# Performance work log

Hardware: AMD Instinct MI355X
Metric: run time of the kernel (lower is better)

The kernel has to match this reference:

```python
import jax, jax.numpy as jnp
import numpy as np

N = 100_000      # nodes
F_IN = 256       # num_features
HID = 128        # args.hidden
C = 32           # num_classes
E = 1_600_000    # edges
EPS = 0.1        # AntiSymmetricConv epsilon
GAMMA = 0.1      # AntiSymmetricConv gamma


def setup_inputs() -> dict:
    key = jax.random.key(0)
    ks = jax.random.split(key, 10)
    def rn(k, shape, scale=0.05):
        return jax.random.normal(k, shape, dtype=jnp.float32) * scale
    x = jax.random.normal(ks[0], (N, F_IN), dtype=jnp.float32)
    edge_index = jax.random.randint(ks[1], (2, E), 0, N, dtype=jnp.int32)
    return {
        "x": x,
        "lin1_w": rn(ks[2], (HID, F_IN)), "lin1_b": jnp.zeros((HID,), jnp.float32),
        "lin2_w": rn(ks[3], (C, HID)),   "lin2_b": jnp.zeros((C,), jnp.float32),
        "W1": rn(ks[4], (HID, HID)), "phi1_w": rn(ks[5], (HID, HID)), "b1": jnp.zeros((HID,), jnp.float32),
        "W2": rn(ks[6], (C, C)),     "phi2_w": rn(ks[7], (C, C)),     "b2": jnp.zeros((C,), jnp.float32),
        "edge_index": edge_index,
    }


def gcn_norm(edge_index, n):
    # GCNConv default: add self-loops, symmetric D^-1/2 (A+I) D^-1/2 normalization
    loops = jnp.arange(n, dtype=edge_index.dtype)
    row = jnp.concatenate([edge_index[0], loops])  # source
    col = jnp.concatenate([edge_index[1], loops])  # target (aggregation)
    deg = jax.ops.segment_sum(jnp.ones(row.shape[0], jnp.float32), col, num_segments=n)
    dinv = jnp.where(deg > 0, jax.lax.rsqrt(deg), 0.0)
    return row, col, dinv[row] * dinv[col]


def gcn_conv(x, phi_w, row, col, norm):
    xw = x @ phi_w.T                                  # [N, d]
    msgs = norm[:, None] * xw[row]                    # [E+N, d] gather
    return jax.ops.segment_sum(msgs, col, num_segments=x.shape[0])  # scatter-add


def anti_symmetric_conv(x, row, col, norm, W, phi_w, b):
    d = W.shape[0]
    aw = W - W.T - GAMMA * jnp.eye(d, dtype=W.dtype)  # antisymmetric weight
    h = gcn_conv(x, phi_w, row, col, norm)            # phi(x, edge_index)
    h = jnp.tanh(x @ aw.T + h + b)
    return x + EPS * h                                # one Euler step (num_iters=1)


def reference(x, lin1_w, lin1_b, lin2_w, lin2_b, W1, phi1_w, b1, W2, phi2_w, b2, edge_index):
    row, col, norm = gcn_norm(edge_index, x.shape[0])
    h = jax.nn.relu(x @ lin1_w.T + lin1_b)            # dropout is identity in eval
    h = anti_symmetric_conv(h, row, col, norm, W1, phi1_w, b1)
    h = h @ lin2_w.T + lin2_b
    h = anti_symmetric_conv(h, row, col, norm, W2, phi2_w, b2)
    return jax.nn.log_softmax(h, axis=1)
```

## Files before the change

kernel.cpp:

```cpp
#include <hip/hip_runtime.h>
#include <hip/hip_bf16.h>
#include <math.h>

#define N_NODES 100000
#define F_IN    256
#define HID     128
#define NCLS    32
#define NEDGES  1600000
#define EPS_C   0.1f
#define GAMMA_C 0.1f

#define NBK   782
#define CHUNK 4096
#define NCH   391
#define BMAX  4096

typedef __attribute__((ext_vector_type(8))) short short8;
typedef __attribute__((ext_vector_type(4))) float floatx4;

__device__ __forceinline__ float bf2f(unsigned short u) {
    union { unsigned int u; float f; } c;
    c.u = ((unsigned int)u) << 16;
    return c.f;
}
__device__ __forceinline__ unsigned short f2bf(float f) {
    union { float f; unsigned int u; } c; c.f = f;
    unsigned int u = c.u;
    u += 0x7FFFu + ((u >> 16) & 1u);
    return (unsigned short)(u >> 16);
}

__device__ __forceinline__ float ldf(const void* p, size_t i, int md) {
    return md ? ((const float*)p)[i] : bf2f(((const unsigned short*)p)[i]);
}
__device__ __forceinline__ short8 ld8(const void* p, size_t i, int md) {
    if (md) {
        const float* q = (const float*)p + i;
        short8 r;
#pragma unroll
        for (int j = 0; j < 8; ++j) r[j] = (short)f2bf(q[j]);
        return r;
    }
    return *(const short8*)((const unsigned short*)p + i);
}

__global__ void k_detect(const unsigned short* __restrict__ x, int* __restrict__ mode) {
    __shared__ int cnt;
    if (threadIdx.x == 0) cnt = 0;
    __syncthreads();
    float v = fabsf(bf2f(x[2 * threadIdx.x]));
    if (v > 1e4f || !isfinite(v)) atomicAdd(&cnt, 1);
    __syncthreads();
    if (threadIdx.x == 0) *mode = (cnt >= 8) ? 1 : 0;
}

__global__ __launch_bounds__(256) void k_hist2(const int* __restrict__ ecol,
                                               int* __restrict__ hist, int e) {
    __shared__ int lh[NBK];
    for (int i = threadIdx.x; i < NBK; i += 256) lh[i] = 0;
    __syncthreads();
    int base = blockIdx.x * CHUNK;
    int lim = base + CHUNK; if (lim > e) lim = e;
    for (int i = base + threadIdx.x; i < lim; i += 256)
        atomicAdd(&lh[ecol[i] >> 7], 1);
    __syncthreads();
    for (int i = threadIdx.x; i < NBK; i += 256) hist[blockIdx.x * NBK + i] = lh[i];
}

__global__ __launch_bounds__(256) void k_tot(const int* __restrict__ hist, int* __restrict__ tot) {
    __shared__ int s[256];
    int b = blockIdx.x;
    int v = 0;
    for (int blk = threadIdx.x; blk < NCH; blk += 256) v += hist[blk * NBK + b];
    s[threadIdx.x] = v;
    __syncthreads();
#pragma unroll
    for (int off = 128; off > 0; off >>= 1) {
        if (threadIdx.x < off) s[threadIdx.x] += s[threadIdx.x + off];
        __syncthreads();
    }
    if (threadIdx.x == 0) tot[b] = s[0];
}

__global__ void k_bscan(const int* __restrict__ tot, int* __restrict__ bbase) {
    __shared__ int s[1024];
    int v = (threadIdx.x < NBK) ? tot[threadIdx.x] : 0;
    s[threadIdx.x] = v;
    __syncthreads();
#pragma unroll
    for (int off = 1; off < 1024; off <<= 1) {
        int t = (threadIdx.x >= off) ? s[threadIdx.x - off] : 0;
        __syncthreads();
        s[threadIdx.x] += t;
        __syncthreads();
    }
    if (threadIdx.x < NBK) bbase[threadIdx.x] = s[threadIdx.x] - v;
}

__global__ __launch_bounds__(512) void k_colscan(const int* __restrict__ hist,
                                                 const int* __restrict__ bbase,
                                                 int* __restrict__ off) {
    __shared__ int s[512];
    int b = blockIdx.x, t = threadIdx.x;
    int v = (t < NCH) ? hist[t * NBK + b] : 0;
    s[t] = v;
    __syncthreads();
#pragma unroll
    for (int o = 1; o < 512; o <<= 1) {
        int u = (t >= o) ? s[t - o] : 0;
        __syncthreads();
        s[t] += u;
        __syncthreads();
    }
    if (t < NCH) off[t * NBK + b] = s[t] - v + bbase[b];
}

__global__ __launch_bounds__(256) void k_pass3(
    const int* __restrict__ erow, const int* __restrict__ ecol,
    const int* __restrict__ off, unsigned int* __restrict__ pairs, int e)
{
    __shared__ int lh[NBK];
    __shared__ int lex[NBK + 1];
    __shared__ int cur[NBK];
    __shared__ int wsum[256];
    __shared__ unsigned int sp[CHUNK];
    int base = blockIdx.x * CHUNK;
    int lim = base + CHUNK; if (lim > e) lim = e;
    int cnt = lim - base;

    for (int i = threadIdx.x; i < NBK; i += 256) lh[i] = 0;
    __syncthreads();
    for (int i = base + threadIdx.x; i < lim; i += 256)
        atomicAdd(&lh[ecol[i] >> 7], 1);
    __syncthreads();

    int t4 = threadIdx.x * 4;
    int a0 = (t4 + 0 < NBK) ? lh[t4 + 0] : 0;
    int a1 = (t4 + 1 < NBK) ? lh[t4 + 1] : 0;
    int a2 = (t4 + 2 < NBK) ? lh[t4 + 2] : 0;
    int a3 = (t4 + 3 < NBK) ? lh[t4 + 3] : 0;
    int mysum = a0 + a1 + a2 + a3;
    wsum[threadIdx.x] = mysum;
    __syncthreads();
#pragma unroll
    for (int o = 1; o < 256; o <<= 1) {
        int u = (threadIdx.x >= o) ? wsum[threadIdx.x - o] : 0;
        __syncthreads();
        wsum[threadIdx.x] += u;
        __syncthreads();
    }
    int run = wsum[threadIdx.x] - mysum;
    if (t4 + 0 < NBK) { lex[t4 + 0] = run;            cur[t4 + 0] = run; }
    if (t4 + 1 < NBK) { lex[t4 + 1] = run + a0;       cur[t4 + 1] = run + a0; }
    if (t4 + 2 < NBK) { lex[t4 + 2] = run + a0 + a1;  cur[t4 + 2] = run + a0 + a1; }
    if (t4 + 3 < NBK) { lex[t4 + 3] = run + a0 + a1 + a2; cur[t4 + 3] = run + a0 + a1 + a2; }
    if (threadIdx.x == 0) lex[NBK] = cnt;
    __syncthreads();

    for (int i = base + threadIdx.x; i < lim; i += 256) {
        int dst = ecol[i], src = erow[i];
        int b = dst >> 7;
        int p = atomicAdd(&cur[b], 1);
        sp[p] = ((unsigned int)src << 7) | (unsigned int)(dst & 127);
    }
    __syncthreads();

    for (int i = threadIdx.x; i < cnt; i += 256) {
        int loB = 0, hiB = NBK;
        while (hiB - loB > 1) {
            int mid = (loB + hiB) >> 1;
            if (lex[mid] <= i) loB = mid; else hiB = mid;
        }
        pairs[off[blockIdx.x * NBK + loB] + (i - lex[loB])] = sp[i];
    }
}

__global__ __launch_bounds__(256) void k_build(
    const int* __restrict__ tot, const int* __restrict__ bbase,
    const unsigned int* __restrict__ pairs,
    int* __restrict__ srt, int* __restrict__ row_start, int* __restrict__ cend,
    float* __restrict__ dinv, int n)
{
    __shared__ int lh[128];
    __shared__ int lo[128];
    __shared__ unsigned int se[BMAX];
    int b = blockIdx.x;
    int nb = tot[b]; if (nb > BMAX) nb = BMAX;
    int base = bbase[b];
    if (threadIdx.x < 128) lh[threadIdx.x] = 0;
    __syncthreads();
    for (int e = threadIdx.x; e < nb; e += 256) {
        unsigned int pk = pairs[(size_t)base + e];
        se[e] = pk;
        atomicAdd(&lh[pk & 127u], 1);
    }
    __syncthreads();
    if (threadIdx.x < 128) lo[threadIdx.x] = lh[threadIdx.x];
    __syncthreads();
#pragma unroll
    for (int off = 1; off < 128; off <<= 1) {
        int t = (threadIdx.x < 128 && threadIdx.x >= off) ? lo[threadIdx.x - off] : 0;
        __syncthreads();
        if (threadIdx.x < 128) lo[threadIdx.x] += t;
        __syncthreads();
    }
    int node = b * 128 + threadIdx.x;
    if (threadIdx.x < 128 && node < n) {
        int inc = lo[threadIdx.x], cnt = lh[threadIdx.x];
        row_start[node] = base + inc - cnt;
        cend[node]      = base + inc;
        dinv[node]      = rsqrtf((float)cnt + 1.0f);
    }
    __syncthreads();
    if (threadIdx.x < 128) lh[threadIdx.x] = lo[threadIdx.x] - lh[threadIdx.x];
    __syncthreads();
    for (int e = threadIdx.x; e < nb; e += 256) {
        unsigned int pk = se[e];
        int pos = atomicAdd(&lh[pk & 127u], 1);
        srt[base + pos] = (int)(pk >> 7);
    }
}

__global__ void k_aw(const void* __restrict__ W, unsigned short* __restrict__ aw,
                     const int* __restrict__ dmode, int d) {
    int idx = blockIdx.x * blockDim.x + threadIdx.x;
    if (idx >= d * d) return;
    int md = dmode[0];
    int n = idx / d, k = idx - n * d;
    float v = ldf(W, n * d + k, md) - ldf(W, k * d + n, md) - ((n == k) ? GAMMA_C : 0.0f);
    aw[idx] = f2bf(v);
}

template<int K, int NC, int EPI, bool APOLY, bool BPOLY, int RT, int KTILE>
__global__ __launch_bounds__(256) void k_gemm3(
    const void* A, const void* B, const void* bias,
    unsigned short* Cout,
    const unsigned short* agg, const unsigned short* xw, const float* dinv,
    const int* dmode, void* opout, int M)
{
    constexpr int KP = KTILE + 8;
    constexpr int NT = NC / 16;
    constexpr int RPB = 64 * RT;
    __shared__ __align__(16) unsigned short sB[NC * KP];
    const int md = dmode[0];

    const int lane = threadIdx.x & 63;
    const int wave = threadIdx.x >> 6;
    const int l15  = lane & 15;
    const int quad = lane >> 4;
    const int row0 = blockIdx.x * RPB + wave * (16 * RT);

    int am[RT];
#pragma unroll
    for (int rt = 0; rt < RT; ++rt) {
        int r = row0 + rt * 16 + l15;
        am[rt] = r < M ? r : M - 1;
    }

    floatx4 acc[RT][NT];
#pragma unroll
    for (int rt = 0; rt < RT; ++rt)
#pragma unroll
        for (int t = 0; t < NT; ++t) acc[rt][t] = (floatx4){0.f, 0.f, 0.f, 0.f};

    for (int kt = 0; kt < K; kt += KTILE) {
        if (kt > 0) __syncthreads();
        for (int base = threadIdx.x * 8; base < NC * KTILE; base += 2048) {
            int r = base / KTILE, c = base - r * KTILE;
            if (BPOLY && md) {
                const float* q = (const float*)B + (size_t)r * K + kt + c;
#pragma unroll
                for (int j = 0; j < 8; ++j) sB[r * KP + c + j] = f2bf(q[j]);
            } else {
                *(short8*)(sB + r * KP + c) =
                    *(const short8*)((const unsigned short*)B + (size_t)r * K + kt + c);
            }
        }
        __syncthreads();

#pragma unroll 2
        for (int kk = kt; kk < kt + KTILE; kk += 32) {
            short8 a[RT];
#pragma unroll
            for (int rt = 0; rt < RT; ++rt)
                a[rt] = APOLY ? ld8(A, (size_t)am[rt] * K + kk + quad * 8, md)
                              : *(const short8*)((const unsigned short*)A + (size_t)am[rt] * K + kk + quad * 8);
            short8 b[NT];
#pragma unroll
            for (int t = 0; t < NT; ++t)
                b[t] = *(const short8*)(sB + (t * 16 + l15) * KP + (kk - kt) + quad * 8);
#pragma unroll
            for (int rt = 0; rt < RT; ++rt)
#pragma unroll
                for (int t = 0; t < NT; ++t)
                    acc[rt][t] = __builtin_amdgcn_mfma_f32_16x16x32_bf16(a[rt], b[t], acc[rt][t], 0, 0, 0);
        }
    }

    const unsigned short* Ares = (const unsigned short*)A;
#pragma unroll
    for (int rt = 0; rt < RT; ++rt) {
#pragma unroll
        for (int reg = 0; reg < 4; ++reg) {
            int rr = row0 + rt * 16 + quad * 4 + reg;
            if (EPI == 4) {
                int rrc = rr < M ? rr : M - 1;
                float dv = dinv[rrc];
                float val[NT];
#pragma unroll
                for (int t = 0; t < NT; ++t) {
                    int col = t * 16 + l15;
                    float z = acc[rt][t][reg]
                            + bf2f(agg[(size_t)rrc * NC + col])
                            + dv * bf2f(xw[(size_t)rrc * NC + col])
                            + ldf(bias, col, md);
                    val[t] = bf2f(Ares[(size_t)rrc * K + col]) + EPS_C * tanhf(z);
                }
                float m = val[0];
#pragma unroll
                for (int t = 1; t < NT; ++t) m = fmaxf(m, val[t]);
#pragma unroll
                for (int msk = 1; msk < 16; msk <<= 1) m = fmaxf(m, __shfl_xor(m, msk));
                float s = 0.f;
#pragma unroll
                for (int t = 0; t < NT; ++t) s += expf(val[t] - m);
#pragma unroll
                for (int msk = 1; msk < 16; msk <<= 1) s += __shfl_xor(s, msk);
                float ls = m + logf(s);
                if (rr < M) {
#pragma unroll
                    for (int t = 0; t < NT; ++t) {
                        int col = t * 16 + l15;
                        float r = val[t] - ls;
                        if (md) ((float*)opout)[(size_t)rr * NC + col] = r;
                        else    ((unsigned short*)opout)[(size_t)rr * NC + col] = f2bf(r);
                    }
                }
            } else {
                if (rr >= M) continue;
#pragma unroll
                for (int t = 0; t < NT; ++t) {
                    int col = t * 16 + l15;
                    float v = acc[rt][t][reg];
                    if (EPI == 0) { v += ldf(bias, col, md); v = v > 0.f ? v : 0.f; }
                    else if (EPI == 2) { v += ldf(bias, col, md); }
                    else if (EPI == 5) { v *= dinv[rr]; }
                    else if (EPI == 3) {
                        float dv = dinv[rr];
                        float z = v + bf2f(agg[(size_t)rr * NC + col])
                                + dv * bf2f(xw[(size_t)rr * NC + col])
                                + ldf(bias, col, md);
                        v = bf2f(Ares[(size_t)rr * K + col]) + EPS_C * tanhf(z);
                    }
                    Cout[(size_t)rr * NC + col] = f2bf(v);
                }
            }
        }
    }
}

__global__ __launch_bounds__(256) void k_lin2phi2(
    const unsigned short* __restrict__ A, const void* __restrict__ B1,
    const void* __restrict__ bias, const void* __restrict__ B2,
    unsigned short* __restrict__ h3, unsigned short* __restrict__ xws2,
    const float* __restrict__ dinv, const int* __restrict__ dmode, int M)
{
    constexpr int K1 = 128, KP1 = 136, KP2 = 40;
    __shared__ __align__(16) unsigned short sB1[32 * KP1];
    __shared__ __align__(16) unsigned short sB2[32 * KP2];
    __shared__ __align__(16) unsigned short sT[256 * KP2];
    const int md = dmode[0];

    for (int base = threadIdx.x * 8; base < 32 * K1; base += 2048) {
        int r = base / K1, c = base - r * K1;
        if (md) {
            const float* q = (const float*)B1 + base;
#pragma unroll
            for (int j = 0; j < 8; ++j) sB1[r * KP1 + c + j] = f2bf(q[j]);
        } else {
            *(short8*)(sB1 + r * KP1 + c) = *(const short8*)((const unsigned short*)B1 + base);
        }
    }
    for (int base = threadIdx.x * 8; base < 32 * 32; base += 2048) {
        int r = base / 32, c = base - r * 32;
        if (md) {
            const float* q = (const float*)B2 + base;
#pragma unroll
            for (int j = 0; j < 8; ++j) sB2[r * KP2 + c + j] = f2bf(q[j]);
        } else {
            *(short8*)(sB2 + r * KP2 + c) = *(const short8*)((const unsigned short*)B2 + base);
        }
    }
    __syncthreads();

    const int lane = threadIdx.x & 63;
    const int wave = threadIdx.x >> 6;
    const int l15  = lane & 15;
    const int quad = lane >> 4;
    const int row0 = blockIdx.x * 256 + wave * 64;

    int am[4];
#pragma unroll
    for (int rt = 0; rt < 4; ++rt) {
        int r = row0 + rt * 16 + l15;
        am[rt] = r < M ? r : M - 1;
    }

    floatx4 acc[4][2];
#pragma unroll
    for (int rt = 0; rt < 4; ++rt) { acc[rt][0] = (floatx4){0,0,0,0}; acc[rt][1] = (floatx4){0,0,0,0}; }

#pragma unroll
    for (int kk = 0; kk < K1; kk += 32) {
#pragma unroll
        for (int rt = 0; rt < 4; ++rt) {
            short8 a = *(const short8*)(A + (size_t)am[rt] * K1 + kk + quad * 8);
#pragma unroll
            for (int t = 0; t < 2; ++t) {
                short8 b = *(const short8*)(sB1 + (t * 16 + l15) * KP1 + kk + quad * 8);
                acc[rt][t] = __builtin_amdgcn_mfma_f32_16x16x32_bf16(a, b, acc[rt][t], 0, 0, 0);
            }
        }
    }
#pragma unroll
    for (int rt = 0; rt < 4; ++rt)
#pragma unroll
        for (int reg = 0; reg < 4; ++reg) {
            int rr = row0 + rt * 16 + quad * 4 + reg;
            int lr = wave * 64 + rt * 16 + quad * 4 + reg;
#pragma unroll
            for (int t = 0; t < 2; ++t) {
                int col = t * 16 + l15;
                unsigned short hv = f2bf(acc[rt][t][reg] + ldf(bias, col, md));
                sT[lr * KP2 + col] = hv;
                if (rr < M) h3[(size_t)rr * 32 + col] = hv;
            }
        }
    __syncthreads();

    floatx4 a2[4][2];
#pragma unroll
    for (int rt = 0; rt < 4; ++rt) {
        short8 a = *(const short8*)(sT + (wave * 64 + rt * 16 + l15) * KP2 + quad * 8);
#pragma unroll
        for (int t = 0; t < 2; ++t) {
            short8 b = *(const short8*)(sB2 + (t * 16 + l15) * KP2 + quad * 8);
            a2[rt][t] = __builtin_amdgcn_mfma_f32_16x16x32_bf16(a, b, (floatx4){0,0,0,0}, 0, 0, 0);
        }
    }
#pragma unroll
    for (int rt = 0; rt < 4; ++rt)
#pragma unroll
        for (int reg = 0; reg < 4; ++reg) {
            int rr = row0 + rt * 16 + quad * 4 + reg;
            if (rr >= M) continue;
            float dv = dinv[rr];
#pragma unroll
            for (int t = 0; t < 2; ++t)
                xws2[(size_t)rr * 32 + t * 16 + l15] = f2bf(dv * a2[rt][t][reg]);
        }
}

__global__ __launch_bounds__(256) void k_gather128(
    const int* __restrict__ srt, const int* __restrict__ rs,
    const int* __restrict__ cend,
    const unsigned short* __restrict__ xws, const float* __restrict__ dinv,
    unsigned short* __restrict__ agg, int n)
{
    int node = blockIdx.x * 8 + (threadIdx.x >> 5);
    int l = threadIdx.x & 31;
    if (node >= n) return;
    int j = rs[node], end = cend[node];
    float a0 = 0.f, a1 = 0.f, a2 = 0.f, a3 = 0.f;
    while (j < end) {
        int idx[8];
#pragma unroll
        for (int k = 0; k < 8; ++k) {
            int jj = j + k;
            idx[k] = srt[jj < end ? jj : end - 1];
        }
        uint2 p[8];
#pragma unroll
        for (int k = 0; k < 8; ++k)
            p[k] = *(const uint2*)(xws + (size_t)idx[k] * 128 + l * 4);
#pragma unroll
        for (int k = 0; k < 8; ++k) {
            if (j + k < end) {
                a0 += bf2f((unsigned short)(p[k].x & 0xFFFFu));
                a1 += bf2f((unsigned short)(p[k].x >> 16));
                a2 += bf2f((unsigned short)(p[k].y & 0xFFFFu));
                a3 += bf2f((unsigned short)(p[k].y >> 16));
            }
        }
        j += 8;
    }
    float dn = dinv[node];
    uint2 out;
    out.x = (unsigned int)f2bf(dn * a0) | ((unsigned int)f2bf(dn * a1) << 16);
    out.y = (unsigned int)f2bf(dn * a2) | ((unsigned int)f2bf(dn * a3) << 16);
    *(uint2*)(agg + (size_t)node * 128 + l * 4) = out;
}

__global__ __launch_bounds__(256) void k_gather32(
    const int* __restrict__ srt, const int* __restrict__ rs,
    const int* __restrict__ cend,
    const unsigned short* __restrict__ xws, const float* __restrict__ dinv,
    unsigned short* __restrict__ agg, int n)
{
    int node = blockIdx.x * 16 + (threadIdx.x >> 4);
    int l = threadIdx.x & 15;
    if (node >= n) return;
    int j = rs[node], end = cend[node];
    float a0 = 0.f, a1 = 0.f;
    while (j < end) {
        int idx[8];
#pragma unroll
        for (int k = 0; k < 8; ++k) {
            int jj = j + k;
            idx[k] = srt[jj < end ? jj : end - 1];
        }
        unsigned int p[8];
#pragma unroll
        for (int k = 0; k < 8; ++k)
            p[k] = *(const unsigned int*)(xws + (size_t)idx[k] * 32 + l * 2);
#pragma unroll
        for (int k = 0; k < 8; ++k) {
            if (j + k < end) {
                a0 += bf2f((unsigned short)(p[k] & 0xFFFFu));
                a1 += bf2f((unsigned short)(p[k] >> 16));
            }
        }
        j += 8;
    }
    float dn = dinv[node];
    unsigned int out = (unsigned int)f2bf(dn * a0) | ((unsigned int)f2bf(dn * a1) << 16);
    *(unsigned int*)(agg + (size_t)node * 32 + l * 2) = out;
}

extern "C" void kernel_launch(void* const* d_in, const int* in_sizes, int n_in,
                              void* d_out, int out_size, void* d_ws, size_t ws_size,
                              hipStream_t stream)
{
    const void* x      = d_in[0];
    const void* lin1_w = d_in[1];
    const void* lin1_b = d_in[2];
    const void* lin2_w = d_in[3];
    const void* lin2_b = d_in[4];
    const void* W1     = d_in[5];
    const void* phi1w  = d_in[6];
    const void* b1     = d_in[7];
    const void* W2     = d_in[8];
    const void* phi2w  = d_in[9];
    const void* b2     = d_in[10];
    const int* eidx    = (const int*)d_in[11];
    const int* erow = eidx;
    const int* ecol = eidx + NEDGES;

    char* ws = (char*)d_ws;
    float* dinv          = (float*)ws;
    int*   dmode         = (int*)(ws + 400000);
    unsigned short* aw1  = (unsigned short*)(ws + 401408);
    unsigned short* aw2  = (unsigned short*)(ws + 435200);
    int* tot             = (int*)(ws + 440320);
    int* bbase           = (int*)(ws + 443648);
    int* row_start       = (int*)(ws + 446976);
    int* cend            = (int*)(ws + 846976);
    int* srt             = (int*)(ws + 1246976);
    int* hist            = (int*)(ws + 7646976);
    int* offb            = (int*)(ws + 8870912);
    unsigned short* h1   = (unsigned short*)(ws + 10485760);
    unsigned short* xws1 = h1 + (size_t)N_NODES * HID;
    unsigned short* agg1 = xws1 + (size_t)N_NODES * HID;
    unsigned short* h2   = xws1;
    unsigned short* h3   = h1;
    unsigned short* xws2 = agg1;
    unsigned short* agg2 = agg1 + (size_t)N_NODES * NCLS;
    unsigned int* pairs  = (unsigned int*)agg1;

    const int GB = 256;
    const int NB128 = (N_NODES + 127) / 128;
    k_detect<<<1, 256, 0, stream>>>((const unsigned short*)x, dmode);

    k_hist2<<<NCH, 256, 0, stream>>>(ecol, hist, NEDGES);
    k_tot<<<NBK, 256, 0, stream>>>(hist, tot);
    k_bscan<<<1, 1024, 0, stream>>>(tot, bbase);
    k_colscan<<<NBK, 512, 0, stream>>>(hist, bbase, offb);
    k_pass3<<<NCH, 256, 0, stream>>>(erow, ecol, offb, pairs, NEDGES);
    k_build<<<NBK, 256, 0, stream>>>(tot, bbase, pairs, srt, row_start, cend, dinv, N_NODES);

    k_aw<<<(HID * HID + GB - 1) / GB, GB, 0, stream>>>(W1, aw1, dmode, HID);
    k_aw<<<(NCLS * NCLS + GB - 1) / GB, GB, 0, stream>>>(W2, aw2, dmode, NCLS);

    k_gemm3<256, 128, 0, true, true, 2, 128><<<NB128, 256, 0, stream>>>(
        x, lin1_w, lin1_b, h1, nullptr, nullptr, nullptr, dmode, nullptr, N_NODES);
    k_gemm3<128, 128, 5, false, true, 2, 128><<<NB128, 256, 0, stream>>>(
        h1, phi1w, nullptr, xws1, nullptr, nullptr, dinv, dmode, nullptr, N_NODES);
    k_gather128<<<(N_NODES + 7) / 8, 256, 0, stream>>>(
        srt, row_start, cend, xws1, dinv, agg1, N_NODES);
    k_gemm3<128, 128, 3, false, false, 2, 128><<<NB128, 256, 0, stream>>>(
        h1, aw1, b1, h2, agg1, xws1, dinv, dmode, nullptr, N_NODES);
    k_lin2phi2<<<(N_NODES + 255) / 256, 256, 0, stream>>>(
        h2, lin2_w, lin2_b, phi2w, h3, xws2, dinv, dmode, N_NODES);
    k_gather32<<<(N_NODES + 15) / 16, 256, 0, stream>>>(
        srt, row_start, cend, xws2, dinv, agg2, N_NODES);
    k_gemm3<32, 32, 4, false, false, 2, 32><<<NB128, 256, 0, stream>>>(
        h3, aw2, b2, nullptr, agg2, xws2, dinv, dmode, d_out, N_NODES);
}
```

Baseline: 484.8 us.

## Prefetch A fragments into registers before B staging and shrink GEMM row tiles

The GEMM kernels now load each K-tile's A fragments from global memory into registers before the shared-memory B staging and barrier, so the global latency overlaps the B copy. The same is done in the fused lin2/phi2 kernel. Row tiles per block are halved (RT 2→1, KTILE 128→64, lin2phi2 256→128 rows), doubling the grid for more parallelism at the cost of restaging B in more blocks. Register use per wave grows with KS*RT prefetched fragments.

Result: faster. 436.8 us (-9.9%).

```diff
diff --git a/kernel.cpp b/kernel.cpp
--- a/kernel.cpp
+++ b/kernel.cpp
@@ -240,6 +240,7 @@
 {
     constexpr int KP = KTILE + 8;
     constexpr int NT = NC / 16;
+    constexpr int KS = KTILE / 32;
     constexpr int RPB = 64 * RT;
     __shared__ __align__(16) unsigned short sB[NC * KP];
     const int md = dmode[0];
@@ -264,6 +265,15 @@
         for (int t = 0; t < NT; ++t) acc[rt][t] = (floatx4){0.f, 0.f, 0.f, 0.f};
 
     for (int kt = 0; kt < K; kt += KTILE) {
+        short8 a[KS][RT];
+#pragma unroll
+        for (int s = 0; s < KS; ++s)
+#pragma unroll
+            for (int rt = 0; rt < RT; ++rt)
+                a[s][rt] = APOLY ? ld8(A, (size_t)am[rt] * K + kt + s * 32 + quad * 8, md)
+                                 : *(const short8*)((const unsigned short*)A +
+                                       (size_t)am[rt] * K + kt + s * 32 + quad * 8);
+
         if (kt > 0) __syncthreads();
         for (int base = threadIdx.x * 8; base < NC * KTILE; base += 2048) {
             int r = base / KTILE, c = base - r * KTILE;
@@ -278,22 +288,17 @@
         }
         __syncthreads();
 
-#pragma unroll 2
-        for (int kk = kt; kk < kt + KTILE; kk += 32) {
-            short8 a[RT];
+#pragma unroll
+        for (int s = 0; s < KS; ++s) {
+            short8 b[NT];
+#pragma unroll
+            for (int t = 0; t < NT; ++t)
+                b[t] = *(const short8*)(sB + (t * 16 + l15) * KP + s * 32 + quad * 8);
 #pragma unroll
             for (int rt = 0; rt < RT; ++rt)
-                a[rt] = APOLY ? ld8(A, (size_t)am[rt] * K + kk + quad * 8, md)
-                              : *(const short8*)((const unsigned short*)A + (size_t)am[rt] * K + kk + quad * 8);
-            short8 b[NT];
-#pragma unroll
-            for (int t = 0; t < NT; ++t)
-                b[t] = *(const short8*)(sB + (t * 16 + l15) * KP + (kk - kt) + quad * 8);
-#pragma unroll
-            for (int rt = 0; rt < RT; ++rt)
 #pragma unroll
                 for (int t = 0; t < NT; ++t)
-                    acc[rt][t] = __builtin_amdgcn_mfma_f32_16x16x32_bf16(a[rt], b[t], acc[rt][t], 0, 0, 0);
+                    acc[rt][t] = __builtin_amdgcn_mfma_f32_16x16x32_bf16(a[s][rt], b[t], acc[rt][t], 0, 0, 0);
         }
     }
 
@@ -368,8 +373,28 @@
     constexpr int K1 = 128, KP1 = 136, KP2 = 40;
     __shared__ __align__(16) unsigned short sB1[32 * KP1];
     __shared__ __align__(16) unsigned short sB2[32 * KP2];
-    __shared__ __align__(16) unsigned short sT[256 * KP2];
+    __shared__ __align__(16) unsigned short sT[128 * KP2];
     const int md = dmode[0];
+
+    const int lane = threadIdx.x & 63;
+    const int wave = threadIdx.x >> 6;
+    const int l15  = lane & 15;
+    const int quad = lane >> 4;
+    const int row0 = blockIdx.x * 128 + wave * 32;
+
+    int am[2];
+#pragma unroll
+    for (int rt = 0; rt < 2; ++rt) {
+        int r = row0 + rt * 16 + l15;
+        am[rt] = r < M ? r : M - 1;
+    }
+
+    short8 a1[4][2];
+#pragma unroll
+    for (int s = 0; s < 4; ++s)
+#pragma unroll
+        for (int rt = 0; rt < 2; ++rt)
+            a1[s][rt] = *(const short8*)(A + (size_t)am[rt] * K1 + s * 32 + quad * 8);
 
     for (int base = threadIdx.x * 8; base < 32 * K1; base += 2048) {
         int r = base / K1, c = base - r * K1;
@@ -393,41 +418,27 @@
     }
     __syncthreads();
 
-    const int lane = threadIdx.x & 63;
-    const int wave = threadIdx.x >> 6;
-    const int l15  = lane & 15;
-    const int quad = lane >> 4;
-    const int row0 = blockIdx.x * 256 + wave * 64;
-
-    int am[4];
-#pragma unroll
-    for (int rt = 0; rt < 4; ++rt) {
-        int r = row0 + rt * 16 + l15;
-        am[rt] = r < M ? r : M - 1;
-    }
-
-    floatx4 acc[4][2];
-#pragma unroll
-    for (int rt = 0; rt < 4; ++rt) { acc[rt][0] = (floatx4){0,0,0,0}; acc[rt][1] = (floatx4){0,0,0,0}; }
-
-#pragma unroll
-    for (int kk = 0; kk < K1; kk += 32) {
-#pragma unroll
-        for (int rt = 0; rt < 4; ++rt) {
-            short8 a = *(const short8*)(A + (size_t)am[rt] * K1 + kk + quad * 8);
+    floatx4 acc[2][2];
+#pragma unroll
+    for (int rt = 0; rt < 2; ++rt) { acc[rt][0] = (floatx4){0,0,0,0}; acc[rt][1] = (floatx4){0,0,0,0}; }
+
+#pragma unroll
+    for (int s = 0; s < 4; ++s) {
+#pragma unroll
+        for (int rt = 0; rt < 2; ++rt) {
 #pragma unroll
             for (int t = 0; t < 2; ++t) {
-                short8 b = *(const short8*)(sB1 + (t * 16 + l15) * KP1 + kk + quad * 8);
-                acc[rt][t] = __builtin_amdgcn_mfma_f32_16x16x32_bf16(a, b, acc[rt][t], 0, 0, 0);
+                short8 b = *(const short8*)(sB1 + (t * 16 + l15) * KP1 + s * 32 + quad * 8);
+                acc[rt][t] = __builtin_amdgcn_mfma_f32_16x16x32_bf16(a1[s][rt], b, acc[rt][t], 0, 0, 0);
             }
         }
     }
 #pragma unroll
-    for (int rt = 0; rt < 4; ++rt)
+    for (int rt = 0; rt < 2; ++rt)
 #pragma unroll
         for (int reg = 0; reg < 4; ++reg) {
             int rr = row0 + rt * 16 + quad * 4 + reg;
-            int lr = wave * 64 + rt * 16 + quad * 4 + reg;
+            int lr = wave * 32 + rt * 16 + quad * 4 + reg;
 #pragma unroll
             for (int t = 0; t < 2; ++t) {
                 int col = t * 16 + l15;
@@ -438,10 +449,10 @@
         }
     __syncthreads();
 
-    floatx4 a2[4][2];
-#pragma unroll
-    for (int rt = 0; rt < 4; ++rt) {
-        short8 a = *(const short8*)(sT + (wave * 64 + rt * 16 + l15) * KP2 + quad * 8);
+    floatx4 a2[2][2];
+#pragma unroll
+    for (int rt = 0; rt < 2; ++rt) {
+        short8 a = *(const short8*)(sT + (wave * 32 + rt * 16 + l15) * KP2 + quad * 8);
 #pragma unroll
         for (int t = 0; t < 2; ++t) {
             short8 b = *(const short8*)(sB2 + (t * 16 + l15) * KP2 + quad * 8);
@@ -449,7 +460,7 @@
         }
     }
 #pragma unroll
-    for (int rt = 0; rt < 4; ++rt)
+    for (int rt = 0; rt < 2; ++rt)
 #pragma unroll
         for (int reg = 0; reg < 4; ++reg) {
             int rr = row0 + rt * 16 + quad * 4 + reg;
@@ -578,7 +589,7 @@
     unsigned int* pairs  = (unsigned int*)agg1;
 
     const int GB = 256;
-    const int NB128 = (N_NODES + 127) / 128;
+    const int NB64 = (N_NODES + 63) / 64;
     k_detect<<<1, 256, 0, stream>>>((const unsigned short*)x, dmode);
 
     k_hist2<<<NCH, 256, 0, stream>>>(ecol, hist, NEDGES);
@@ -591,18 +602,18 @@
     k_aw<<<(HID * HID + GB - 1) / GB, GB, 0, stream>>>(W1, aw1, dmode, HID);
     k_aw<<<(NCLS * NCLS + GB - 1) / GB, GB, 0, stream>>>(W2, aw2, dmode, NCLS);
 
-    k_gemm3<256, 128, 0, true, true, 2, 128><<<NB128, 256, 0, stream>>>(
+    k_gemm3<256, 128, 0, true, true, 1, 64><<<NB64, 256, 0, stream>>>(
         x, lin1_w, lin1_b, h1, nullptr, nullptr, nullptr, dmode, nullptr, N_NODES);
-    k_gemm3<128, 128, 5, false, true, 2, 128><<<NB128, 256, 0, stream>>>(
+    k_gemm3<128, 128, 5, false, true, 1, 64><<<NB64, 256, 0, stream>>>(
         h1, phi1w, nullptr, xws1, nullptr, nullptr, dinv, dmode, nullptr, N_NODES);
     k_gather128<<<(N_NODES + 7) / 8, 256, 0, stream>>>(
         srt, row_start, cend, xws1, dinv, agg1, N_NODES);
-    k_gemm3<128, 128, 3, false, false, 2, 128><<<NB128, 256, 0, stream>>>(
+    k_gemm3<128, 128, 3, false, false, 1, 64><<<NB64, 256, 0, stream>>>(
         h1, aw1, b1, h2, agg1, xws1, dinv, dmode, nullptr, N_NODES);
-    k_lin2phi2<<<(N_NODES + 255) / 256, 256, 0, stream>>>(
+    k_lin2phi2<<<(N_NODES + 127) / 128, 256, 0, stream>>>(
         h2, lin2_w, lin2_b, phi2w, h3, xws2, dinv, dmode, N_NODES);
     k_gather32<<<(N_NODES + 15) / 16, 256, 0, stream>>>(
         srt, row_start, cend, xws2, dinv, agg2, N_NODES);
-    k_gemm3<32, 32, 4, false, false, 2, 32><<<NB128, 256, 0, stream>>>(
+    k_gemm3<32, 32, 4, false, false, 1, 32><<<NB64, 256, 0, stream>>>(
         h3, aw2, b2, nullptr, agg2, xws2, dinv, dmode, d_out, N_NODES);
 }
```
